# Kernel tuning notes

Hardware: AMD Instinct MI355X
Metric: run time of the kernel (lower is better)

Reference implementation:

```python
import jax, jax.numpy as jnp
import numpy as np

MODES = 128
NEG_SLOPE = 0.2


def setup_inputs() -> dict:
    key = jax.random.key(0)
    k1, k2 = jax.random.split(key)
    x = jax.random.normal(k1, (32, 256, 4096), dtype=jnp.float32)
    weight = jax.random.normal(k2, (256, 256, MODES, 2), dtype=jnp.float32)
    return {"x": x, "weight": weight}


def reference(x, weight):
    B, C, M = x.shape
    n_freq = M // 2 + 1
    n_modes = min(MODES, n_freq)  # static
    # rfft along last dim -> (B, C, n_freq) complex64
    x_ft = jnp.fft.rfft(x, axis=-1)
    # complex per-mode mixing weight: (C_out, C_in, modes)
    w = weight[..., 0] + 1j * weight[..., 1]
    # out_ft[b,o,m] = sum_i x_ft[b,i,m] * w[o,i,m]  (batched complex GEMM over modes)
    out_low = jnp.einsum('bim,oim->bom', x_ft[:, :, :n_modes], w[:, :, :n_modes])
    # zero-fill the remaining frequencies
    out_ft = jnp.concatenate(
        [out_low, jnp.zeros((B, C, n_freq - n_modes), dtype=out_low.dtype)], axis=-1)
    x_ifft = jnp.fft.irfft(out_ft, n=M, axis=-1)
    # LeakyReLU(0.2) then residual add
    return x + jnp.where(x_ifft >= 0, x_ifft, NEG_SLOPE * x_ifft)
```

## Files before the change

kernel.cpp:

```cpp
#include <hip/hip_runtime.h>


typedef unsigned short u16;
typedef unsigned int   u32;
typedef __attribute__((ext_vector_type(8))) short bf16x8;
typedef __attribute__((ext_vector_type(4))) float f32x4;

#define MLEN  4096

__device__ __forceinline__ u16 f2b(float f) {
  u32 u = __float_as_uint(f);
  u += 0x7fffu + ((u >> 16) & 1u);
  return (u16)(u >> 16);
}
__device__ __forceinline__ float blo(u32 p) { return __uint_as_float(p << 16); }
__device__ __forceinline__ float bhi(u32 p) { return __uint_as_float(p & 0xffff0000u); }

__global__ void probe_kernel(const u16* __restrict__ x16, int* __restrict__ flag) {
  __shared__ int cnt;
  if (threadIdx.x == 0) cnt = 0;
  __syncthreads();
  int c = 0;
  for (int j = threadIdx.x; j < 4096; j += 256) {
    u32 e = (x16[j] >> 7) & 0xFFu;
    if (e >= 0x8Fu) ++c;
  }
  atomicAdd(&cnt, c);
  __syncthreads();
  if (threadIdx.x == 0) flag[0] = (cnt > 256) ? 0 : 1;
}

__global__ void basis_kernel(u16* __restrict__ Bas1P, u16* __restrict__ Bas2P) {
  int t = blockIdx.x;
  int c = threadIdx.x;
  {
    int p = c >> 7, rem = c & 127, j = rem >> 1, s2 = rem & 1;
    int m = 2 * j + p;
    int idx = (m * t) & 4095;
    float theta = (float)idx * (6.283185307179586f / 4096.0f);
    float s, cth;
    __sincosf(theta, &s, &cth);
    Bas2P[t * 256 + c] = f2b(s2 ? -s : cth);
  }
  {
    int parity = c >> 7, isim = (c >> 6) & 1, j = c & 63;
    int m = 2 * j + parity;
    int idx = (m * t) & 4095;
    float theta = (float)idx * (6.283185307179586f / 4096.0f);
    float s, cth;
    __sincosf(theta, &s, &cth);
    Bas1P[c * 2048 + t] = f2b(isim ? -s : cth);
  }
}

template <int BM, int BN, int EPI, bool ADUAL>
__global__ __launch_bounds__(256)
void gemm_nt(const void* __restrict__ A, const u16* __restrict__ Bt,
             int K, int lda, int ldb,
             u32* __restrict__ Xp, int ldc,
             const void* __restrict__ xres, void* __restrict__ outp,
             const int* __restrict__ flag) {
  constexpr int LD = 72;
  constexpr int FM = BM / 32;
  constexpr int FN = BN / 32;
  __shared__ __align__(16) char smem[(BM + BN) * LD * 2];
  u16* As = (u16*)smem;
  u16* Bs = (u16*)(smem + BM * LD * 2);
  const int mode = (ADUAL || EPI == 1) ? flag[0] : 1;
  const int tid = threadIdx.x;
  const int bn0 = blockIdx.x * BN;
  const int bm0 = blockIdx.y * BM;
  const int lane = tid & 63;
  const int wave = tid >> 6;
  const int wm = wave >> 1, wn = wave & 1;
  const int l15 = lane & 15, q4 = lane >> 4;

  const u16* Btb = Bt;
  if constexpr (EPI == 2) Btb += (size_t)blockIdx.z * BN * ldb;

  f32x4 acc[FM][FN] = {};
  f32x4 acc2[FM][FN] = {};

  auto kstep = [&](f32x4 (&ac)[FM][FN]) {
#pragma unroll
    for (int kk = 0; kk < 2; ++kk) {
      const int ko = kk * 32 + q4 * 8;
      bf16x8 af[FM], bfr[FN];
#pragma unroll
      for (int mi = 0; mi < FM; ++mi)
        af[mi] = *(const bf16x8*)&As[(wm * (BM / 2) + mi * 16 + l15) * LD + ko];
#pragma unroll
      for (int ni = 0; ni < FN; ++ni)
        bfr[ni] = *(const bf16x8*)&Bs[(wn * (BN / 2) + ni * 16 + l15) * LD + ko];
#pragma unroll
      for (int mi = 0; mi < FM; ++mi)
#pragma unroll
        for (int ni = 0; ni < FN; ++ni)
          ac[mi][ni] = __builtin_amdgcn_mfma_f32_16x16x32_bf16(
              af[mi], bfr[ni], ac[mi][ni], 0, 0, 0);
    }
  };

  for (int kt = 0; kt < K; kt += 64) {
    __syncthreads();
    if constexpr (EPI == 2) {
      const int neg = blockIdx.z;
#pragma unroll
      for (int q = tid; q < BM * 8; q += 256) {
        int row = q >> 3, c8 = q & 7;
        u16 tmp[8];
        if (mode == 1) {
          const u16* s0 = &((const u16*)A)[(size_t)(bm0 + row) * lda + kt + c8 * 8];
          uint4 a0 = *(const uint4*)s0;
          uint4 a1 = *(const uint4*)(s0 + 2048);
          u32 aw[4] = {a0.x, a0.y, a0.z, a0.w};
          u32 bw[4] = {a1.x, a1.y, a1.z, a1.w};
#pragma unroll
          for (int j = 0; j < 4; ++j) {
            float lo = neg ? (blo(aw[j]) - blo(bw[j])) : (blo(aw[j]) + blo(bw[j]));
            float hi = neg ? (bhi(aw[j]) - bhi(bw[j])) : (bhi(aw[j]) + bhi(bw[j]));
            tmp[2 * j]     = f2b(lo);
            tmp[2 * j + 1] = f2b(hi);
          }
        } else {
          const float* s0 = &((const float*)A)[(size_t)(bm0 + row) * lda + kt + c8 * 8];
          float4 f0 = *(const float4*)s0;
          float4 f1 = *(const float4*)(s0 + 4);
          float4 g0 = *(const float4*)(s0 + 2048);
          float4 g1 = *(const float4*)(s0 + 2052);
          float a[8] = {f0.x, f0.y, f0.z, f0.w, f1.x, f1.y, f1.z, f1.w};
          float b[8] = {g0.x, g0.y, g0.z, g0.w, g1.x, g1.y, g1.z, g1.w};
#pragma unroll
          for (int j = 0; j < 8; ++j)
            tmp[j] = f2b(neg ? (a[j] - b[j]) : (a[j] + b[j]));
        }
        *(uint4*)&As[row * LD + c8 * 8] = *(const uint4*)tmp;
      }
    } else {
      const u16* Ab = (const u16*)A;
#pragma unroll
      for (int q = tid; q < BM * 8; q += 256) {
        int row = q >> 3, c8 = q & 7;
        *(uint4*)&As[row * LD + c8 * 8] =
            *(const uint4*)&Ab[(size_t)(bm0 + row) * lda + kt + c8 * 8];
      }
    }
#pragma unroll
    for (int q = tid; q < BN * 8; q += 256) {
      int row = q >> 3, c8 = q & 7;
      *(uint4*)&Bs[row * LD + c8 * 8] =
          *(const uint4*)&Btb[(size_t)(bn0 + row) * ldb + kt + c8 * 8];
    }
    __syncthreads();
    if constexpr (EPI == 1) {
      if (kt >= 128) kstep(acc2); else kstep(acc);
    } else {
      kstep(acc);
    }
  }

  if constexpr (EPI == 1) {
    float* Cs = (float*)smem;
    const int s = tid >> 3;
    const int c8 = tid & 7;
#pragma unroll
    for (int mi = 0; mi < FM; ++mi) {
      __syncthreads();
#pragma unroll
      for (int ni = 0; ni < FN; ++ni) {
        float* dst = &Cs[(wm * 16 + q4 * 4) * 136 + wn * 32 + ni * 16 + l15];
#pragma unroll
        for (int r = 0; r < 4; ++r) {
          float e = acc[mi][ni][r], o = acc2[mi][ni][r];
          dst[r * 136]      = e + o;
          dst[r * 136 + 68] = e - o;
        }
      }
      __syncthreads();
      const int gr = bm0 + mi * 16 + s + ((s < 16) ? 0 : (BM / 2 - 16));
      if (mode == 1) {
        const u16* xr16 = (const u16*)xres;
        u16* o16 = (u16*)outp;
#pragma unroll
        for (int h = 0; h < 2; ++h) {
          float4 va = *(const float4*)&Cs[s * 136 + h * 68 + c8 * 8];
          float4 vb = *(const float4*)&Cs[s * 136 + h * 68 + c8 * 8 + 4];
          size_t gidx = (size_t)gr * ldc + bn0 + h * 2048 + c8 * 8;
          uint4 xv = *(const uint4*)&xr16[gidx];
          float cv[8] = {va.x, va.y, va.z, va.w, vb.x, vb.y, vb.z, vb.w};
          u32 xw[4] = {xv.x, xv.y, xv.z, xv.w};
          u16 ov[8];
#pragma unroll
          for (int j = 0; j < 4; ++j) {
            float l0 = cv[2 * j]     >= 0.f ? cv[2 * j]     : 0.2f * cv[2 * j];
            float l1 = cv[2 * j + 1] >= 0.f ? cv[2 * j + 1] : 0.2f * cv[2 * j + 1];
            ov[2 * j]     = f2b(blo(xw[j]) + l0);
            ov[2 * j + 1] = f2b(bhi(xw[j]) + l1);
          }
          *(uint4*)&o16[gidx] = *(const uint4*)ov;
        }
      } else {
        const float* xf = (const float*)xres;
        float* of = (float*)outp;
#pragma unroll
        for (int h = 0; h < 2; ++h) {
          float4 v0 = *(const float4*)&Cs[s * 136 + h * 68 + c8 * 8];
          float4 v1 = *(const float4*)&Cs[s * 136 + h * 68 + c8 * 8 + 4];
          size_t gidx = (size_t)gr * ldc + bn0 + h * 2048 + c8 * 8;
          float4 x0 = *(const float4*)&xf[gidx];
          float4 x1 = *(const float4*)&xf[gidx + 4];
          float4 o0, o1;
          o0.x = x0.x + (v0.x >= 0.f ? v0.x : 0.2f * v0.x);
          o0.y = x0.y + (v0.y >= 0.f ? v0.y : 0.2f * v0.y);
          o0.z = x0.z + (v0.z >= 0.f ? v0.z : 0.2f * v0.z);
          o0.w = x0.w + (v0.w >= 0.f ? v0.w : 0.2f * v0.w);
          o1.x = x1.x + (v1.x >= 0.f ? v1.x : 0.2f * v1.x);
          o1.y = x1.y + (v1.y >= 0.f ? v1.y : 0.2f * v1.y);
          o1.z = x1.z + (v1.z >= 0.f ? v1.z : 0.2f * v1.z);
          o1.w = x1.w + (v1.w >= 0.f ? v1.w : 0.2f * v1.w);
          *(float4*)&of[gidx] = o0;
          *(float4*)&of[gidx + 4] = o1;
        }
      }
    }
  } else {
    constexpr int LP = 136;
    u16* Ls = (u16*)smem;
    __syncthreads();
#pragma unroll
    for (int ni = 0; ni < FN; ++ni) {
      u16* dst = &Ls[(wm * 16 + q4 * 4) * LP + wn * 64 + ni * 16 + l15];
#pragma unroll
      for (int r = 0; r < 4; ++r) dst[r * LP] = f2b(acc[0][ni][r]);
    }
    __syncthreads();
    const int b   = bm0 >> 8;
    const int ic0 = bm0 & 255;
    const int j   = tid & 63, ich = tid >> 6;
    const int woff = (b & 1) * 2 + blockIdx.z;
    const int bp   = b >> 1;
#pragma unroll
    for (int i2 = 0; i2 < 8; ++i2) {
      int ic = i2 * 4 + ich;
      u32 v = (u32)Ls[ic * LP + j] | ((u32)Ls[ic * LP + 64 + j] << 16);
      Xp[((((size_t)(ic0 + ic) * 16 + bp) * 64 + j) << 2) + woff] = v;
    }
  }
}

__global__ __launch_bounds__(1024)
void mix_kernel(const u32* __restrict__ Xp, const void* __restrict__ w,
                u16* __restrict__ Yp, const int* __restrict__ flag) {
  const int tid = threadIdx.x;
  const int wave = tid >> 6, lane = tid & 63;
  const int o = blockIdx.x * 2 + (wave >> 3);
  const int bp = blockIdx.y * 8 + (wave & 7);
  const int m = lane * 2;
  const int mode = flag[0];

  const uint4* X4 = (const uint4*)Xp + (size_t)bp * 64 + lane;

  float ar[2][2] = {}, ai[2][2] = {};

  if (mode == 0) {
    const float* wb = (const float*)w + 2u * ((size_t)o * 32768 + m);
#pragma unroll 8
    for (int ic = 0; ic < 256; ++ic) {
      float4 wp = *(const float4*)&wb[(size_t)ic * 256];
      uint4 xv = X4[(size_t)ic * 1024];
      float wr0 = wp.x, wi0 = wp.y, wr1 = wp.z, wi1 = wp.w;
      float xr, xi;
      xr = blo(xv.x); xi = bhi(xv.x);
      ar[0][0] = fmaf(xr, wr0, fmaf(-xi, wi0, ar[0][0]));
      ai[0][0] = fmaf(xr, wi0, fmaf(xi, wr0, ai[0][0]));
      xr = blo(xv.y); xi = bhi(xv.y);
      ar[0][1] = fmaf(xr, wr1, fmaf(-xi, wi1, ar[0][1]));
      ai[0][1] = fmaf(xr, wi1, fmaf(xi, wr1, ai[0][1]));
      xr = blo(xv.z); xi = bhi(xv.z);
      ar[1][0] = fmaf(xr, wr0, fmaf(-xi, wi0, ar[1][0]));
      ai[1][0] = fmaf(xr, wi0, fmaf(xi, wr0, ai[1][0]));
      xr = blo(xv.w); xi = bhi(xv.w);
      ar[1][1] = fmaf(xr, wr1, fmaf(-xi, wi1, ar[1][1]));
      ai[1][1] = fmaf(xr, wi1, fmaf(xi, wr1, ai[1][1]));
    }
  } else {
    const u32* wb = (const u32*)w + (size_t)o * 32768 + m;
#pragma unroll 8
    for (int ic = 0; ic < 256; ++ic) {
      uint2 wp = *(const uint2*)&wb[(size_t)ic * 128];
      uint4 xv = X4[(size_t)ic * 1024];
      float wr0 = blo(wp.x), wi0 = bhi(wp.x), wr1 = blo(wp.y), wi1 = bhi(wp.y);
      float xr, xi;
      xr = blo(xv.x); xi = bhi(xv.x);
      ar[0][0] = fmaf(xr, wr0, fmaf(-xi, wi0, ar[0][0]));
      ai[0][0] = fmaf(xr, wi0, fmaf(xi, wr0, ai[0][0]));
      xr = blo(xv.y); xi = bhi(xv.y);
      ar[0][1] = fmaf(xr, wr1, fmaf(-xi, wi1, ar[0][1]));
      ai[0][1] = fmaf(xr, wi1, fmaf(xi, wr1, ai[0][1]));
      xr = blo(xv.z); xi = bhi(xv.z);
      ar[1][0] = fmaf(xr, wr0, fmaf(-xi, wi0, ar[1][0]));
      ai[1][0] = fmaf(xr, wi0, fmaf(xi, wr0, ai[1][0]));
      xr = blo(xv.w); xi = bhi(xv.w);
      ar[1][1] = fmaf(xr, wr1, fmaf(-xi, wi1, ar[1][1]));
      ai[1][1] = fmaf(xr, wi1, fmaf(xi, wr1, ai[1][1]));
    }
  }

  const float sIm = 2.0f / 4096.0f;
  const float sRe0 = (m == 0) ? (1.0f / 4096.0f) : (2.0f / 4096.0f);
  const float sRe1 = 2.0f / 4096.0f;
  u32* Yp32 = (u32*)Yp;
#pragma unroll
  for (int jb = 0; jb < 2; ++jb) {
    int b = bp * 2 + jb;
    size_t base = ((size_t)(b * 256 + o)) * 128;
    u32 we = (u32)f2b(ar[jb][0] * sRe0) | ((u32)f2b(ai[jb][0] * sIm) << 16);
    u32 wo = (u32)f2b(ar[jb][1] * sRe1) | ((u32)f2b(ai[jb][1] * sIm) << 16);
    Yp32[base + lane] = we;
    Yp32[base + 64 + lane] = wo;
  }
}

extern "C" void kernel_launch(void* const* d_in, const int* in_sizes, int n_in,
                              void* d_out, int out_size, void* d_ws, size_t ws_size,
                              hipStream_t stream) {
  const void* x = d_in[0];
  const void* w = d_in[1];

  char* ws = (char*)d_ws;
  int*  flag  = (int*)(ws);
  u16*  Bas1P = (u16*)(ws + (1u << 20));
  u16*  Bas2P = (u16*)(ws + (2u << 20));
  u32*  Xp4   = (u32*)(ws + (4u << 20));
  u16*  Yp    = (u16*)(ws + (8u << 20));

  probe_kernel<<<dim3(1), dim3(256), 0, stream>>>((const u16*)x, flag);
  basis_kernel<<<dim3(2048), dim3(256), 0, stream>>>(Bas1P, Bas2P);

  gemm_nt<32, 128, 2, true><<<dim3(1, 256, 2), dim3(256), 0, stream>>>(
      x, Bas1P, 2048, MLEN, 2048, Xp4, 0, nullptr, nullptr, flag);

  mix_kernel<<<dim3(128, 2), dim3(1024), 0, stream>>>(Xp4, w, Yp, flag);

  gemm_nt<128, 64, 1, false><<<dim3(32, 64, 1), dim3(256), 0, stream>>>(
      Yp, Bas2P, 256, 256, 256, nullptr, MLEN, x, d_out, flag);
}
```

Measured before the change: 457.4 us.

## Register-prefetch next K tile in GEMM and double-buffer loads in mix kernel

The GEMM main loop now loads the next 64-wide K tile of A and B into registers while the MFMA step runs on the current shared-memory tile, then writes it to LDS at the top of the next iteration. The mix kernel's channel loop is restructured into two register buffers of four channels each, so loads for one chunk are issued before the other chunk is computed. Both aim to hide global memory latency behind compute, at the cost of more registers and possibly lower occupancy. In the EPI==2 path the prefetch assumes BM*8 equals 256, so one row chunk per thread.

```diff
diff --git a/kernel.cpp b/kernel.cpp
--- a/kernel.cpp
+++ b/kernel.cpp
@@ -63,6 +63,8 @@
   constexpr int LD = 72;
   constexpr int FM = BM / 32;
   constexpr int FN = BN / 32;
+  constexpr int AITER = (BM * 8) / 256;
+  constexpr int BITER = (BN * 8) / 256;
   __shared__ __align__(16) char smem[(BM + BN) * LD * 2];
   u16* As = (u16*)smem;
   u16* Bs = (u16*)(smem + BM * LD * 2);
@@ -81,6 +83,77 @@
   f32x4 acc[FM][FN] = {};
   f32x4 acc2[FM][FN] = {};
 
+  uint4  aU[AITER];
+  uint4  a16b;
+  float4 af0, af1, ag0, ag1;
+  uint4  bU[BITER];
+
+  auto stage_load = [&](int kt) {
+    if constexpr (EPI == 2) {
+      const int row = tid >> 3, c8 = tid & 7;
+      if (mode == 1) {
+        const u16* s0 = &((const u16*)A)[(size_t)(bm0 + row) * lda + kt + c8 * 8];
+        aU[0] = *(const uint4*)s0;
+        a16b  = *(const uint4*)(s0 + 2048);
+      } else {
+        const float* s0 = &((const float*)A)[(size_t)(bm0 + row) * lda + kt + c8 * 8];
+        af0 = *(const float4*)s0;
+        af1 = *(const float4*)(s0 + 4);
+        ag0 = *(const float4*)(s0 + 2048);
+        ag1 = *(const float4*)(s0 + 2052);
+      }
+    } else {
+      const u16* Ab = (const u16*)A;
+#pragma unroll
+      for (int i = 0; i < AITER; ++i) {
+        int q = tid + i * 256, row = q >> 3, c8 = q & 7;
+        aU[i] = *(const uint4*)&Ab[(size_t)(bm0 + row) * lda + kt + c8 * 8];
+      }
+    }
+#pragma unroll
+    for (int i = 0; i < BITER; ++i) {
+      int q = tid + i * 256, row = q >> 3, c8 = q & 7;
+      bU[i] = *(const uint4*)&Btb[(size_t)(bn0 + row) * ldb + kt + c8 * 8];
+    }
+  };
+
+  auto stage_store = [&]() {
+    if constexpr (EPI == 2) {
+      const int row = tid >> 3, c8 = tid & 7;
+      const int neg = blockIdx.z;
+      u16 tmp[8];
+      if (mode == 1) {
+        u32 aw[4] = {aU[0].x, aU[0].y, aU[0].z, aU[0].w};
+        u32 bw[4] = {a16b.x, a16b.y, a16b.z, a16b.w};
+#pragma unroll
+        for (int j = 0; j < 4; ++j) {
+          float lo = neg ? (blo(aw[j]) - blo(bw[j])) : (blo(aw[j]) + blo(bw[j]));
+          float hi = neg ? (bhi(aw[j]) - bhi(bw[j])) : (bhi(aw[j]) + bhi(bw[j]));
+          tmp[2 * j]     = f2b(lo);
+          tmp[2 * j + 1] = f2b(hi);
+        }
+      } else {
+        float a[8] = {af0.x, af0.y, af0.z, af0.w, af1.x, af1.y, af1.z, af1.w};
+        float b[8] = {ag0.x, ag0.y, ag0.z, ag0.w, ag1.x, ag1.y, ag1.z, ag1.w};
+#pragma unroll
+        for (int j = 0; j < 8; ++j)
+          tmp[j] = f2b(neg ? (a[j] - b[j]) : (a[j] + b[j]));
+      }
+      *(uint4*)&As[row * LD + c8 * 8] = *(const uint4*)tmp;
+    } else {
+#pragma unroll
+      for (int i = 0; i < AITER; ++i) {
+        int q = tid + i * 256, row = q >> 3, c8 = q & 7;
+        *(uint4*)&As[row * LD + c8 * 8] = aU[i];
+      }
+    }
+#pragma unroll
+    for (int i = 0; i < BITER; ++i) {
+      int q = tid + i * 256, row = q >> 3, c8 = q & 7;
+      *(uint4*)&Bs[row * LD + c8 * 8] = bU[i];
+    }
+  };
+
   auto kstep = [&](f32x4 (&ac)[FM][FN]) {
 #pragma unroll
     for (int kk = 0; kk < 2; ++kk) {
@@ -101,57 +174,12 @@
     }
   };
 
+  stage_load(0);
   for (int kt = 0; kt < K; kt += 64) {
     __syncthreads();
-    if constexpr (EPI == 2) {
-      const int neg = blockIdx.z;
-#pragma unroll
-      for (int q = tid; q < BM * 8; q += 256) {
-        int row = q >> 3, c8 = q & 7;
-        u16 tmp[8];
-        if (mode == 1) {
-          const u16* s0 = &((const u16*)A)[(size_t)(bm0 + row) * lda + kt + c8 * 8];
-          uint4 a0 = *(const uint4*)s0;
-          uint4 a1 = *(const uint4*)(s0 + 2048);
-          u32 aw[4] = {a0.x, a0.y, a0.z, a0.w};
-          u32 bw[4] = {a1.x, a1.y, a1.z, a1.w};
-#pragma unroll
-          for (int j = 0; j < 4; ++j) {
-            float lo = neg ? (blo(aw[j]) - blo(bw[j])) : (blo(aw[j]) + blo(bw[j]));
-            float hi = neg ? (bhi(aw[j]) - bhi(bw[j])) : (bhi(aw[j]) + bhi(bw[j]));
-            tmp[2 * j]     = f2b(lo);
-            tmp[2 * j + 1] = f2b(hi);
-          }
-        } else {
-          const float* s0 = &((const float*)A)[(size_t)(bm0 + row) * lda + kt + c8 * 8];
-          float4 f0 = *(const float4*)s0;
-          float4 f1 = *(const float4*)(s0 + 4);
-          float4 g0 = *(const float4*)(s0 + 2048);
-          float4 g1 = *(const float4*)(s0 + 2052);
-          float a[8] = {f0.x, f0.y, f0.z, f0.w, f1.x, f1.y, f1.z, f1.w};
-          float b[8] = {g0.x, g0.y, g0.z, g0.w, g1.x, g1.y, g1.z, g1.w};
-#pragma unroll
-          for (int j = 0; j < 8; ++j)
-            tmp[j] = f2b(neg ? (a[j] - b[j]) : (a[j] + b[j]));
-        }
-        *(uint4*)&As[row * LD + c8 * 8] = *(const uint4*)tmp;
-      }
-    } else {
-      const u16* Ab = (const u16*)A;
-#pragma unroll
-      for (int q = tid; q < BM * 8; q += 256) {
-        int row = q >> 3, c8 = q & 7;
-        *(uint4*)&As[row * LD + c8 * 8] =
-            *(const uint4*)&Ab[(size_t)(bm0 + row) * lda + kt + c8 * 8];
-      }
-    }
-#pragma unroll
-    for (int q = tid; q < BN * 8; q += 256) {
-      int row = q >> 3, c8 = q & 7;
-      *(uint4*)&Bs[row * LD + c8 * 8] =
-          *(const uint4*)&Btb[(size_t)(bn0 + row) * ldb + kt + c8 * 8];
-    }
+    stage_store();
     __syncthreads();
+    if (kt + 64 < K) stage_load(kt + 64);
     if constexpr (EPI == 1) {
       if (kt >= 128) kstep(acc2); else kstep(acc);
     } else {
@@ -264,45 +292,78 @@
 
   if (mode == 0) {
     const float* wb = (const float*)w + 2u * ((size_t)o * 32768 + m);
-#pragma unroll 8
-    for (int ic = 0; ic < 256; ++ic) {
-      float4 wp = *(const float4*)&wb[(size_t)ic * 256];
-      uint4 xv = X4[(size_t)ic * 1024];
-      float wr0 = wp.x, wi0 = wp.y, wr1 = wp.z, wi1 = wp.w;
-      float xr, xi;
-      xr = blo(xv.x); xi = bhi(xv.x);
-      ar[0][0] = fmaf(xr, wr0, fmaf(-xi, wi0, ar[0][0]));
-      ai[0][0] = fmaf(xr, wi0, fmaf(xi, wr0, ai[0][0]));
-      xr = blo(xv.y); xi = bhi(xv.y);
-      ar[0][1] = fmaf(xr, wr1, fmaf(-xi, wi1, ar[0][1]));
-      ai[0][1] = fmaf(xr, wi1, fmaf(xi, wr1, ai[0][1]));
-      xr = blo(xv.z); xi = bhi(xv.z);
-      ar[1][0] = fmaf(xr, wr0, fmaf(-xi, wi0, ar[1][0]));
-      ai[1][0] = fmaf(xr, wi0, fmaf(xi, wr0, ai[1][0]));
-      xr = blo(xv.w); xi = bhi(xv.w);
-      ar[1][1] = fmaf(xr, wr1, fmaf(-xi, wi1, ar[1][1]));
-      ai[1][1] = fmaf(xr, wi1, fmaf(xi, wr1, ai[1][1]));
+    float4 wA[4], wB[4];
+    uint4  xA[4], xB[4];
+    auto LDC = [&](float4 (&wv)[4], uint4 (&xv)[4], int c) {
+#pragma unroll
+      for (int i = 0; i < 4; ++i) {
+        wv[i] = *(const float4*)&wb[(size_t)(c * 4 + i) * 256];
+        xv[i] = X4[(size_t)(c * 4 + i) * 1024];
+      }
+    };
+    auto CMP = [&](float4 (&wv)[4], uint4 (&xv)[4]) {
+#pragma unroll
+      for (int i = 0; i < 4; ++i) {
+        float wr0 = wv[i].x, wi0 = wv[i].y, wr1 = wv[i].z, wi1 = wv[i].w;
+        float xr, xi;
+        xr = blo(xv[i].x); xi = bhi(xv[i].x);
+        ar[0][0] = fmaf(xr, wr0, fmaf(-xi, wi0, ar[0][0]));
+        ai[0][0] = fmaf(xr, wi0, fmaf(xi, wr0, ai[0][0]));
+        xr = blo(xv[i].y); xi = bhi(xv[i].y);
+        ar[0][1] = fmaf(xr, wr1, fmaf(-xi, wi1, ar[0][1]));
+        ai[0][1] = fmaf(xr, wi1, fmaf(xi, wr1, ai[0][1]));
+        xr = blo(xv[i].z); xi = bhi(xv[i].z);
+        ar[1][0] = fmaf(xr, wr0, fmaf(-xi, wi0, ar[1][0]));
+        ai[1][0] = fmaf(xr, wi0, fmaf(xi, wr0, ai[1][0]));
+        xr = blo(xv[i].w); xi = bhi(xv[i].w);
+        ar[1][1] = fmaf(xr, wr1, fmaf(-xi, wi1, ar[1][1]));
+        ai[1][1] = fmaf(xr, wi1, fmaf(xi, wr1, ai[1][1]));
+      }
+    };
+    LDC(wA, xA, 0);
+    for (int c = 0; c < 64; c += 2) {
+      LDC(wB, xB, c + 1);
+      CMP(wA, xA);
+      if (c + 2 < 64) LDC(wA, xA, c + 2);
+      CMP(wB, xB);
     }
   } else {
     const u32* wb = (const u32*)w + (size_t)o * 32768 + m;
-#pragma unroll 8
-    for (int ic = 0; ic < 256; ++ic) {
-      uint2 wp = *(const uint2*)&wb[(size_t)ic * 128];
-      uint4 xv = X4[(size_t)ic * 1024];
-      float wr0 = blo(wp.x), wi0 = bhi(wp.x), wr1 = blo(wp.y), wi1 = bhi(wp.y);
-      float xr, xi;
-      xr = blo(xv.x); xi = bhi(xv.x);
-      ar[0][0] = fmaf(xr, wr0, fmaf(-xi, wi0, ar[0][0]));
-      ai[0][0] = fmaf(xr, wi0, fmaf(xi, wr0, ai[0][0]));
-      xr = blo(xv.y); xi = bhi(xv.y);
-      ar[0][1] = fmaf(xr, wr1, fmaf(-xi, wi1, ar[0][1]));
-      ai[0][1] = fmaf(xr, wi1, fmaf(xi, wr1, ai[0][1]));
-      xr = blo(xv.z); xi = bhi(xv.z);
-      ar[1][0] = fmaf(xr, wr0, fmaf(-xi, wi0, ar[1][0]));
-      ai[1][0] = fmaf(xr, wi0, fmaf(xi, wr0, ai[1][0]));
-      xr = blo(xv.w); xi = bhi(xv.w);
-      ar[1][1] = fmaf(xr, wr1, fmaf(-xi, wi1, ar[1][1]));
-      ai[1][1] = fmaf(xr, wi1, fmaf(xi, wr1, ai[1][1]));
+    uint2 wA[4], wB[4];
+    uint4 xA[4], xB[4];
+    auto LDC = [&](uint2 (&wv)[4], uint4 (&xv)[4], int c) {
+#pragma unroll
+      for (int i = 0; i < 4; ++i) {
+        wv[i] = *(const uint2*)&wb[(size_t)(c * 4 + i) * 128];
+        xv[i] = X4[(size_t)(c * 4 + i) * 1024];
+      }
+    };
+    auto CMP = [&](uint2 (&wv)[4], uint4 (&xv)[4]) {
+#pragma unroll
+      for (int i = 0; i < 4; ++i) {
+        float wr0 = blo(wv[i].x), wi0 = bhi(wv[i].x);
+        float wr1 = blo(wv[i].y), wi1 = bhi(wv[i].y);
+        float xr, xi;
+        xr = blo(xv[i].x); xi = bhi(xv[i].x);
+        ar[0][0] = fmaf(xr, wr0, fmaf(-xi, wi0, ar[0][0]));
+        ai[0][0] = fmaf(xr, wi0, fmaf(xi, wr0, ai[0][0]));
+        xr = blo(xv[i].y); xi = bhi(xv[i].y);
+        ar[0][1] = fmaf(xr, wr1, fmaf(-xi, wi1, ar[0][1]));
+        ai[0][1] = fmaf(xr, wi1, fmaf(xi, wr1, ai[0][1]));
+        xr = blo(xv[i].z); xi = bhi(xv[i].z);
+        ar[1][0] = fmaf(xr, wr0, fmaf(-xi, wi0, ar[1][0]));
+        ai[1][0] = fmaf(xr, wi0, fmaf(xi, wr0, ai[1][0]));
+        xr = blo(xv[i].w); xi = bhi(xv[i].w);
+        ar[1][1] = fmaf(xr, wr1, fmaf(-xi, wi1, ar[1][1]));
+        ai[1][1] = fmaf(xr, wi1, fmaf(xi, wr1, ai[1][1]));
+      }
+    };
+    LDC(wA, xA, 0);
+    for (int c = 0; c < 64; c += 2) {
+      LDC(wB, xB, c + 1);
+      CMP(wA, xA);
+      if (c + 2 < 64) LDC(wA, xA, c + 2);
+      CMP(wB, xB);
     }
   }
 
```

Result: slower. 511.9 us (+11.9%).

## Replace scalar complex mode-mixing with per-mode bf16 MFMA GEMM

Applied to the files above, without the earlier changes.

The per-mode complex channel mixing, previously done with scalar FMAs per thread, becomes a small GEMM per frequency mode on bf16 MFMA instructions. Real and imaginary parts are split into separate shared-memory tiles, with a sign-flipped imaginary weight copy. The forward GEMM epilogue now writes its output mode-major as (mode, batch, channel) so each mix block can load one mode's 32x256 input tile contiguously. Weights are quantized to bf16 when mode 0 inputs are fp32, and weight reads are strided across modes, which may limit memory efficiency.

```diff
diff --git a/kernel.cpp b/kernel.cpp
--- a/kernel.cpp
+++ b/kernel.cpp
@@ -236,89 +236,115 @@
     __syncthreads();
     const int b   = bm0 >> 8;
     const int ic0 = bm0 & 255;
-    const int j   = tid & 63, ich = tid >> 6;
-    const int woff = (b & 1) * 2 + blockIdx.z;
-    const int bp   = b >> 1;
-#pragma unroll
-    for (int i2 = 0; i2 < 8; ++i2) {
-      int ic = i2 * 4 + ich;
-      u32 v = (u32)Ls[ic * LP + j] | ((u32)Ls[ic * LP + 64 + j] << 16);
-      Xp[((((size_t)(ic0 + ic) * 16 + bp) * 64 + j) << 2) + woff] = v;
-    }
-  }
-}
-
-__global__ __launch_bounds__(1024)
-void mix_kernel(const u32* __restrict__ Xp, const void* __restrict__ w,
-                u16* __restrict__ Yp, const int* __restrict__ flag) {
+    const int j   = tid >> 2;
+    const int icg = tid & 3;
+    const int mo  = 2 * j + blockIdx.z;
+    u32 vals[8];
+#pragma unroll
+    for (int ii = 0; ii < 8; ++ii) {
+      int ic = icg * 8 + ii;
+      vals[ii] = (u32)Ls[ic * LP + j] | ((u32)Ls[ic * LP + 64 + j] << 16);
+    }
+    u32* dst = &Xp[((size_t)mo * 32 + b) * 256 + ic0 + icg * 8];
+    *(uint4*)dst       = *(const uint4*)&vals[0];
+    *(uint4*)(dst + 4) = *(const uint4*)&vals[4];
+  }
+}
+
+__global__ __launch_bounds__(256)
+void mixm_kernel(const u32* __restrict__ Xm, const void* __restrict__ w,
+                 u16* __restrict__ Yp, const int* __restrict__ flag) {
+  constexpr int XL = 264;
+  constexpr int WL = 40;
+  __shared__ u16 Xre[32 * XL];
+  __shared__ u16 Xim[32 * XL];
+  __shared__ u16 Wre[64 * WL];
+  __shared__ u16 Wip[64 * WL];
+  __shared__ u16 Win[64 * WL];
   const int tid = threadIdx.x;
-  const int wave = tid >> 6, lane = tid & 63;
-  const int o = blockIdx.x * 2 + (wave >> 3);
-  const int bp = blockIdx.y * 8 + (wave & 7);
-  const int m = lane * 2;
+  const int m  = blockIdx.x;
+  const int o0 = blockIdx.y * 64;
   const int mode = flag[0];
-
-  const uint4* X4 = (const uint4*)Xp + (size_t)bp * 64 + lane;
-
-  float ar[2][2] = {}, ai[2][2] = {};
-
-  if (mode == 0) {
-    const float* wb = (const float*)w + 2u * ((size_t)o * 32768 + m);
-#pragma unroll 8
-    for (int ic = 0; ic < 256; ++ic) {
-      float4 wp = *(const float4*)&wb[(size_t)ic * 256];
-      uint4 xv = X4[(size_t)ic * 1024];
-      float wr0 = wp.x, wi0 = wp.y, wr1 = wp.z, wi1 = wp.w;
-      float xr, xi;
-      xr = blo(xv.x); xi = bhi(xv.x);
-      ar[0][0] = fmaf(xr, wr0, fmaf(-xi, wi0, ar[0][0]));
-      ai[0][0] = fmaf(xr, wi0, fmaf(xi, wr0, ai[0][0]));
-      xr = blo(xv.y); xi = bhi(xv.y);
-      ar[0][1] = fmaf(xr, wr1, fmaf(-xi, wi1, ar[0][1]));
-      ai[0][1] = fmaf(xr, wi1, fmaf(xi, wr1, ai[0][1]));
-      xr = blo(xv.z); xi = bhi(xv.z);
-      ar[1][0] = fmaf(xr, wr0, fmaf(-xi, wi0, ar[1][0]));
-      ai[1][0] = fmaf(xr, wi0, fmaf(xi, wr0, ai[1][0]));
-      xr = blo(xv.w); xi = bhi(xv.w);
-      ar[1][1] = fmaf(xr, wr1, fmaf(-xi, wi1, ar[1][1]));
-      ai[1][1] = fmaf(xr, wi1, fmaf(xi, wr1, ai[1][1]));
-    }
-  } else {
-    const u32* wb = (const u32*)w + (size_t)o * 32768 + m;
-#pragma unroll 8
-    for (int ic = 0; ic < 256; ++ic) {
-      uint2 wp = *(const uint2*)&wb[(size_t)ic * 128];
-      uint4 xv = X4[(size_t)ic * 1024];
-      float wr0 = blo(wp.x), wi0 = bhi(wp.x), wr1 = blo(wp.y), wi1 = bhi(wp.y);
-      float xr, xi;
-      xr = blo(xv.x); xi = bhi(xv.x);
-      ar[0][0] = fmaf(xr, wr0, fmaf(-xi, wi0, ar[0][0]));
-      ai[0][0] = fmaf(xr, wi0, fmaf(xi, wr0, ai[0][0]));
-      xr = blo(xv.y); xi = bhi(xv.y);
-      ar[0][1] = fmaf(xr, wr1, fmaf(-xi, wi1, ar[0][1]));
-      ai[0][1] = fmaf(xr, wi1, fmaf(xi, wr1, ai[0][1]));
-      xr = blo(xv.z); xi = bhi(xv.z);
-      ar[1][0] = fmaf(xr, wr0, fmaf(-xi, wi0, ar[1][0]));
-      ai[1][0] = fmaf(xr, wi0, fmaf(xi, wr0, ai[1][0]));
-      xr = blo(xv.w); xi = bhi(xv.w);
-      ar[1][1] = fmaf(xr, wr1, fmaf(-xi, wi1, ar[1][1]));
-      ai[1][1] = fmaf(xr, wi1, fmaf(xi, wr1, ai[1][1]));
+  const int lane = tid & 63, wv = tid >> 6;
+  const int l15 = lane & 15, q4 = lane >> 4;
+
+  {
+    const int b = tid >> 3, i0 = (tid & 7) * 32;
+    const uint4* src = (const uint4*)(Xm + ((size_t)m * 32 + b) * 256 + i0);
+#pragma unroll
+    for (int c = 0; c < 8; ++c) {
+      uint4 v = src[c];
+      int i = i0 + c * 4;
+      *(u32*)&Xre[b * XL + i]     = (v.x & 0xffffu) | (v.y << 16);
+      *(u32*)&Xre[b * XL + i + 2] = (v.z & 0xffffu) | (v.w << 16);
+      *(u32*)&Xim[b * XL + i]     = (v.x >> 16) | (v.y & 0xffff0000u);
+      *(u32*)&Xim[b * XL + i + 2] = (v.z >> 16) | (v.w & 0xffff0000u);
+    }
+  }
+
+  f32x4 accRe[2] = {}, accIm[2] = {};
+
+  const int so = tid >> 2;
+  const int sk = (tid & 3) * 8;
+
+  for (int kt = 0; kt < 8; ++kt) {
+    const int k0 = kt * 32;
+    __syncthreads();
+    if (mode == 0) {
+      const float* wp = (const float*)w +
+          (((size_t)(o0 + so) * 256 + (k0 + sk)) * 128 + m) * 2;
+#pragma unroll
+      for (int kk = 0; kk < 8; ++kk) {
+        float2 f = *(const float2*)(wp + (size_t)kk * 256);
+        u16 re = f2b(f.x), im = f2b(f.y);
+        Wre[so * WL + sk + kk] = re;
+        Wip[so * WL + sk + kk] = im;
+        Win[so * WL + sk + kk] = im ^ 0x8000u;
+      }
+    } else {
+      const u32* wp = (const u32*)w +
+          ((size_t)(o0 + so) * 256 + (k0 + sk)) * 128 + m;
+#pragma unroll
+      for (int kk = 0; kk < 8; ++kk) {
+        u32 v = wp[(size_t)kk * 128];
+        u16 re = (u16)v, im = (u16)(v >> 16);
+        Wre[so * WL + sk + kk] = re;
+        Wip[so * WL + sk + kk] = im;
+        Win[so * WL + sk + kk] = im ^ 0x8000u;
+      }
+    }
+    __syncthreads();
+    bf16x8 aRe[2], aIm[2];
+#pragma unroll
+    for (int mi = 0; mi < 2; ++mi) {
+      aRe[mi] = *(const bf16x8*)&Xre[(mi * 16 + l15) * XL + k0 + q4 * 8];
+      aIm[mi] = *(const bf16x8*)&Xim[(mi * 16 + l15) * XL + k0 + q4 * 8];
+    }
+    bf16x8 bRe = *(const bf16x8*)&Wre[(wv * 16 + l15) * WL + q4 * 8];
+    bf16x8 bIp = *(const bf16x8*)&Wip[(wv * 16 + l15) * WL + q4 * 8];
+    bf16x8 bIn = *(const bf16x8*)&Win[(wv * 16 + l15) * WL + q4 * 8];
+#pragma unroll
+    for (int mi = 0; mi < 2; ++mi) {
+      accRe[mi] = __builtin_amdgcn_mfma_f32_16x16x32_bf16(aRe[mi], bRe, accRe[mi], 0, 0, 0);
+      accRe[mi] = __builtin_amdgcn_mfma_f32_16x16x32_bf16(aIm[mi], bIn, accRe[mi], 0, 0, 0);
+      accIm[mi] = __builtin_amdgcn_mfma_f32_16x16x32_bf16(aRe[mi], bIp, accIm[mi], 0, 0, 0);
+      accIm[mi] = __builtin_amdgcn_mfma_f32_16x16x32_bf16(aIm[mi], bRe, accIm[mi], 0, 0, 0);
     }
   }
 
   const float sIm = 2.0f / 4096.0f;
-  const float sRe0 = (m == 0) ? (1.0f / 4096.0f) : (2.0f / 4096.0f);
-  const float sRe1 = 2.0f / 4096.0f;
+  const float sRe = (m == 0) ? (1.0f / 4096.0f) : (2.0f / 4096.0f);
   u32* Yp32 = (u32*)Yp;
-#pragma unroll
-  for (int jb = 0; jb < 2; ++jb) {
-    int b = bp * 2 + jb;
-    size_t base = ((size_t)(b * 256 + o)) * 128;
-    u32 we = (u32)f2b(ar[jb][0] * sRe0) | ((u32)f2b(ai[jb][0] * sIm) << 16);
-    u32 wo = (u32)f2b(ar[jb][1] * sRe1) | ((u32)f2b(ai[jb][1] * sIm) << 16);
-    Yp32[base + lane] = we;
-    Yp32[base + 64 + lane] = wo;
-  }
+  const int o = o0 + wv * 16 + l15;
+  const int word = (m & 1) * 64 + (m >> 1);
+#pragma unroll
+  for (int mi = 0; mi < 2; ++mi)
+#pragma unroll
+    for (int r = 0; r < 4; ++r) {
+      int b = mi * 16 + q4 * 4 + r;
+      u32 val = (u32)f2b(accRe[mi][r] * sRe) | ((u32)f2b(accIm[mi][r] * sIm) << 16);
+      Yp32[((size_t)(b * 256 + o)) * 128 + word] = val;
+    }
 }
 
 extern "C" void kernel_launch(void* const* d_in, const int* in_sizes, int n_in,
@@ -331,16 +357,16 @@
   int*  flag  = (int*)(ws);
   u16*  Bas1P = (u16*)(ws + (1u << 20));
   u16*  Bas2P = (u16*)(ws + (2u << 20));
-  u32*  Xp4   = (u32*)(ws + (4u << 20));
+  u32*  Xm    = (u32*)(ws + (4u << 20));
   u16*  Yp    = (u16*)(ws + (8u << 20));
 
   probe_kernel<<<dim3(1), dim3(256), 0, stream>>>((const u16*)x, flag);
   basis_kernel<<<dim3(2048), dim3(256), 0, stream>>>(Bas1P, Bas2P);
 
   gemm_nt<32, 128, 2, true><<<dim3(1, 256, 2), dim3(256), 0, stream>>>(
-      x, Bas1P, 2048, MLEN, 2048, Xp4, 0, nullptr, nullptr, flag);
-
-  mix_kernel<<<dim3(128, 2), dim3(1024), 0, stream>>>(Xp4, w, Yp, flag);
+      x, Bas1P, 2048, MLEN, 2048, Xm, 0, nullptr, nullptr, flag);
+
+  mixm_kernel<<<dim3(128, 4), dim3(256), 0, stream>>>(Xm, w, Yp, flag);
 
   gemm_nt<128, 64, 1, false><<<dim3(32, 64, 1), dim3(256), 0, stream>>>(
       Yp, Bas2P, 256, 256, 256, nullptr, MLEN, x, d_out, flag);
```

New measurement: 477.2 us. +4.3%, slower.
